# Performance work log

Hardware: AMD Instinct MI355X
Metric: run time of the kernel (lower is better)

Reference implementation:

```python
import jax, jax.numpy as jnp
import numpy as np

B = 4096; NINP = 512; NHID = 2048
NBI = 1; NBO = 8; TOPK = 4; NMRI = 2
BSO = NHID // NBO           # 256 (block_size_out)
ATT_OUT = BSO * 4           # 1024
GRU_NINP = ATT_OUT * NBO    # 8192
BSI = GRU_NINP // NBO       # 1024 (GRU per-block input size)
DK_I = 64                   # inp_att d_k (n_head=1)
NH_M = 4; DK_M = 16; DV_M = 16  # mha heads/dims


def setup_inputs() -> dict:
    key = jax.random.key(0)
    ks = jax.random.split(key, 16)
    r = lambda i, shape, s=0.01: (s * jax.random.normal(ks[i], shape)).astype(jnp.float32)
    return {
        "inp": jax.random.normal(ks[0], (B, NBI * NINP), dtype=jnp.float32),
        "hx": jax.random.normal(ks[1], (B, NHID), dtype=jnp.float32),
        "cx": jax.random.normal(ks[2], (B, NHID), dtype=jnp.float32),
        "step": 0,
        # inp_att (GroupLinear q over NBO blocks; k,v over NMRI write slots; fc out)
        "Wq_i": r(3, (NBO, BSO, DK_I)),
        "Wk_i": r(4, (NMRI, NINP, DK_I)),
        "Wv_i": r(5, (NMRI, NINP, ATT_OUT)),
        "fc_i_w": r(6, (ATT_OUT, ATT_OUT), 0.02),
        "fc_i_b": jnp.zeros((ATT_OUT,), jnp.float32),
        # mha (communication attention among blocks)
        "Wq_m": r(7, (NBO, BSO, NH_M * DK_M)),
        "Wk_m": r(8, (NBO, BSO, NH_M * DK_M)),
        "Wv_m": r(9, (NBO, BSO, NH_M * DV_M)),
        "fc_m_w": r(10, (NH_M * DV_M, BSO), 0.05),
        "fc_m_b": jnp.zeros((BSO,), jnp.float32),
        "gate_m_w": r(11, (NH_M * DV_M, BSO), 0.05),
        "gate_m_b": jnp.zeros((BSO,), jnp.float32),
        # block-diagonal GRU cell (blockified params: only diagonal blocks kept)
        "Wih": r(12, (NBO, 3 * BSO, BSI), 0.02),
        "Whh": r(13, (NBO, 3 * BSO, BSO), 0.02),
        "bih": jnp.zeros((NBO, 3 * BSO), jnp.float32),
        "bhh": jnp.zeros((NBO, 3 * BSO), jnp.float32),
    }


def _forward(inp, hx, cx, Wq_i, Wk_i, Wv_i, fc_i_w, fc_i_b, Wq_m, Wk_m, Wv_m,
             fc_m_w, fc_m_b, gate_m_w, gate_m_b, Wih, Whh, bih, bhh):
    b = inp.shape[0]
    # --- build read slots: slot 0 = zeros (null), slot 1 = input ---
    x = inp.reshape(b, NBI, NINP)
    x = jnp.tile(x, (1, NMRI - 1, 1))
    x = jnp.concatenate([jnp.zeros_like(x[:, :1]), x], axis=1)            # (b, NMRI, ninp)
    hx3 = hx.reshape(b, NBO, BSO)
    # --- inp_att: n_head=1, residual=False (gate_fc unused); Sparse_attention no-op (topk>=len_k) ---
    q = jnp.einsum('bni,nio->bno', hx3, Wq_i)                             # (b, NBO, DK_I)
    k = jnp.einsum('bni,nio->bno', x, Wk_i)                               # (b, NMRI, DK_I)
    v = jnp.einsum('bni,nio->bno', x, Wv_i)                               # (b, NMRI, ATT_OUT)
    iatt = jax.nn.softmax(jnp.einsum('bqd,bkd->bqk', q, k) / float(np.sqrt(DK_I)), axis=-1)
    inp_use = jnp.einsum('bqk,bkv->bqv', iatt, v)                         # (b, NBO, ATT_OUT)
    inp_use = (inp_use @ fc_i_w + fc_i_b).reshape(b, NBO * ATT_OUT)
    # --- top-k block mask: zero out the (NBO-TOPK) blocks most attentive to the null slot ---
    drop_idx = jax.lax.top_k(iatt[:, :, 0], NBO - TOPK)[1]                # (b, NBO-TOPK)
    mask = jnp.ones((b, NBO), inp.dtype).at[jnp.arange(b)[:, None], drop_idx].set(0.0)
    mask = jax.lax.stop_gradient(mask)                                    # mask.detach()
    mask_w = jnp.repeat(mask[:, :, None], BSO, axis=2).reshape(b, NHID)
    # --- block-diagonal GRUCell: h' = (1-z)*n + z*h ---
    x3 = inp_use.reshape(b, NBO, BSI)
    gx = jnp.einsum('bki,koi->bko', x3, Wih) + bih                        # (b, NBO, 3*BSO)
    gh = jnp.einsum('bkj,koj->bko', hx3, Whh) + bhh
    xr, xz, xn = jnp.split(gx, 3, axis=-1)
    hr, hz, hn = jnp.split(gh, 3, axis=-1)
    r = jax.nn.sigmoid(xr + hr)
    z = jax.nn.sigmoid(xz + hz)
    n = jnp.tanh(xn + r * hn)
    h_new = (1.0 - z) * n + z * hx3                                       # (b, NBO, BSO)
    # --- step attention among blocks; blocked_grad = identity fwd, grad*mask bwd ---
    m3 = mask[:, :, None]
    hg = m3 * h_new + jax.lax.stop_gradient((1.0 - m3) * h_new)
    qm = jnp.einsum('bni,nio->bno', hg, Wq_m).reshape(b, NBO, NH_M, DK_M)
    km = jnp.einsum('bni,nio->bno', hg, Wk_m).reshape(b, NBO, NH_M, DK_M)
    vm = jnp.einsum('bni,nio->bno', hg, Wv_m).reshape(b, NBO, NH_M, DV_M)
    am = jax.nn.softmax(jnp.einsum('bqhd,bkhd->bhqk', qm, km) / float(np.sqrt(DK_M)), axis=-1)
    om = jnp.einsum('bhqk,bkhd->bqhd', am, vm).reshape(b, NBO, NH_M * DV_M)
    att = jax.nn.sigmoid(om @ gate_m_w + gate_m_b) * jnp.tanh(om @ fc_m_w + fc_m_b)  # residual=True gating
    h_new = (h_new + att).reshape(b, NHID)
    # --- gated state update (GRU: cx_new = hx_new) ---
    hx_out = mask_w * h_new + (1.0 - mask_w) * hx
    cx_out = mask_w * h_new + (1.0 - mask_w) * cx
    return hx_out, cx_out, mask_w


def reference(inp, hx, cx, step, Wq_i, Wk_i, Wv_i, fc_i_w, fc_i_b, Wq_m, Wk_m, Wv_m,
              fc_m_w, fc_m_b, gate_m_w, gate_m_b, Wih, Whh, bih, bhh):
    del step  # unused by the math
    return _forward(inp, hx, cx, Wq_i, Wk_i, Wv_i, fc_i_w, fc_i_b, Wq_m, Wk_m, Wv_m,
                    fc_m_w, fc_m_b, gate_m_w, gate_m_b, Wih, Whh, bih, bhh)
```

## Files before the change

### kernel.cpp

```cpp
#include <hip/hip_runtime.h>
#include <hip/hip_bf16.h>

#define B_SZ 4096
#define NHID_ 2048

typedef __bf16 bf16x8 __attribute__((ext_vector_type(8)));
typedef float f32x4 __attribute__((ext_vector_type(4)));

__device__ __forceinline__ float sigmoidf_(float x) { return 1.f / (1.f + expf(-x)); }

#define GLDS16(gp, lp) __builtin_amdgcn_global_load_lds( \
    (const __attribute__((address_space(1))) void*)(gp), \
    (__attribute__((address_space(3))) void*)(lp), 16, 0, 0)

__global__ __launch_bounds__(256) void prep_all(
    const float* __restrict__ Wih, const float* __restrict__ fc_i_b,
    const float* __restrict__ bih, __hip_bfloat16* __restrict__ Wihb,
    float* __restrict__ cb,
    const float* __restrict__ inp, __hip_bfloat16* __restrict__ inpb,
    const float* __restrict__ Whh, __hip_bfloat16* __restrict__ Whhb,
    const float* __restrict__ WvBsrc, __hip_bfloat16* __restrict__ WvB,
    const float* __restrict__ fc_i_w, __hip_bfloat16* __restrict__ fcT,
    const float* __restrict__ Wq_m, const float* __restrict__ Wk_m,
    const float* __restrict__ Wv_m, __hip_bfloat16* __restrict__ WmT,
    const float* __restrict__ fc_m_w, const float* __restrict__ gate_m_w,
    __hip_bfloat16* __restrict__ fcgT)
{
    __shared__ float smem[32 * 33];
    const int bid = blockIdx.x;
    const int tid = threadIdx.x;

    if (bid < 6144) {
        long j = bid;
        const float* row = Wih + j * 1024;
        __hip_bfloat16* drow = Wihb + j * 1024;
        int i = tid * 4;
        float4 v = *(const float4*)(row + i);
        __hip_bfloat16 b0 = __float2bfloat16(v.x);
        __hip_bfloat16 b1 = __float2bfloat16(v.y);
        __hip_bfloat16 b2 = __float2bfloat16(v.z);
        __hip_bfloat16 b3 = __float2bfloat16(v.w);
        ushort4 u;
        u.x = *(unsigned short*)&b0; u.y = *(unsigned short*)&b1;
        u.z = *(unsigned short*)&b2; u.w = *(unsigned short*)&b3;
        *(ushort4*)(drow + i) = u;
        float s = fc_i_b[i] * v.x + fc_i_b[i + 1] * v.y +
                  fc_i_b[i + 2] * v.z + fc_i_b[i + 3] * v.w;
#pragma unroll
        for (int off = 32; off > 0; off >>= 1) s += __shfl_xor(s, off, 64);
        if ((tid & 63) == 0) smem[tid >> 6] = s;
        __syncthreads();
        if (tid == 0) cb[j] = smem[0] + smem[1] + smem[2] + smem[3] + bih[j];
    } else if (bid < 10240) {
        long i = (long)(bid - 6144) * 256 + tid;
        const float* src; __hip_bfloat16* dst; long off;
        if (i < 524288)       { src = inp;    dst = inpb; off = i; }
        else if (i < 917504)  { src = Whh;    dst = Whhb; off = i - 524288; }
        else                  { src = WvBsrc; dst = WvB;  off = i - 917504; }
        float4 v = ((const float4*)src)[off];
        __hip_bfloat16 b0 = __float2bfloat16(v.x);
        __hip_bfloat16 b1 = __float2bfloat16(v.y);
        __hip_bfloat16 b2 = __float2bfloat16(v.z);
        __hip_bfloat16 b3 = __float2bfloat16(v.w);
        ushort4 u;
        u.x = *(unsigned short*)&b0; u.y = *(unsigned short*)&b1;
        u.z = *(unsigned short*)&b2; u.w = *(unsigned short*)&b3;
        ((ushort4*)dst)[off] = u;
    } else if (bid < 11264) {
        int lb = bid - 10240;
        int r0 = (lb >> 5) * 32, c0 = (lb & 31) * 32;
        int tx = tid & 31, ty = tid >> 5;
        float (*tile)[33] = (float(*)[33])smem;
#pragma unroll
        for (int i = 0; i < 4; ++i)
            tile[ty + i * 8][tx] = fc_i_w[(long)(r0 + ty + i * 8) * 1024 + c0 + tx];
        __syncthreads();
#pragma unroll
        for (int i = 0; i < 4; ++i)
            fcT[(long)(c0 + ty + i * 8) * 1024 + r0 + tx] =
                __float2bfloat16(tile[tx][ty + i * 8]);
    } else if (bid < 11648) {
        int lb = bid - 11264;
        int z = lb >> 4, rem = lb & 15;
        int by = rem >> 1, bx = rem & 1;
        int which = z >> 3, nb = z & 7;
        const float* src = (which == 0) ? Wq_m : (which == 1) ? Wk_m : Wv_m;
        src += (long)nb * 16384;
        __hip_bfloat16* dst = WmT + (long)nb * 49152 + which * 64 * 256;
        int r0 = by * 32, c0 = bx * 32;
        int tx = tid & 31, ty = tid >> 5;
        float (*tile)[33] = (float(*)[33])smem;
#pragma unroll
        for (int i = 0; i < 4; ++i)
            tile[ty + i * 8][tx] = src[(long)(r0 + ty + i * 8) * 64 + c0 + tx];
        __syncthreads();
#pragma unroll
        for (int i = 0; i < 4; ++i)
            dst[(long)(c0 + ty + i * 8) * 256 + r0 + tx] =
                __float2bfloat16(tile[tx][ty + i * 8]);
    } else {
        int t = (bid - 11648) * 256 + tid;
        int np = t >> 6, k = t & 63;
        int o = (np >> 5) * 16 + (np & 15);
        const float* src = ((np >> 4) & 1) ? gate_m_w : fc_m_w;
        fcgT[t] = __float2bfloat16(src[k * 256 + o]);
    }
}

#define GM_BM 64
#define GM_BN 64
#define GM_BK 16

__global__ __launch_bounds__(256) void gemm_nn(
    const float* __restrict__ A, const float* __restrict__ Bm, float* __restrict__ C,
    int M, int N, int K, int lda, int ldb, int ldc,
    long sA, long sB, long sC)
{
    const int z = blockIdx.z;
    A += (long)z * sA; Bm += (long)z * sB; C += (long)z * sC;
    const int m0 = blockIdx.y * GM_BM;
    const int n0 = blockIdx.x * GM_BN;
    const int tid = threadIdx.x;
    const int tx = tid & 15;
    const int ty = tid >> 4;

    __shared__ float As[GM_BK][GM_BM + 4];
    __shared__ float Bs[GM_BK][GM_BN + 4];

    float acc[4][4] = {};

    for (int k0 = 0; k0 < K; k0 += GM_BK) {
#pragma unroll
        for (int i = 0; i < 4; ++i) {
            int idx = tid + i * 256;
            int r = idx >> 4, c = idx & 15;
            As[c][r] = A[(long)(m0 + r) * lda + k0 + c];
        }
#pragma unroll
        for (int i = 0; i < 4; ++i) {
            int idx = tid + i * 256;
            int r = idx >> 6, c = idx & 63;
            Bs[r][c] = Bm[(long)(k0 + r) * ldb + n0 + c];
        }
        __syncthreads();
#pragma unroll
        for (int kk = 0; kk < GM_BK; ++kk) {
            float4 a4 = *(const float4*)&As[kk][ty * 4];
            float4 b4 = *(const float4*)&Bs[kk][tx * 4];
            float av[4] = {a4.x, a4.y, a4.z, a4.w};
            float bv[4] = {b4.x, b4.y, b4.z, b4.w};
#pragma unroll
            for (int i = 0; i < 4; ++i)
#pragma unroll
                for (int j = 0; j < 4; ++j)
                    acc[i][j] += av[i] * bv[j];
        }
        __syncthreads();
    }
#pragma unroll
    for (int i = 0; i < 4; ++i) {
        long m = m0 + ty * 4 + i;
#pragma unroll
        for (int j = 0; j < 4; ++j) {
            int n = n0 + tx * 4 + j;
            C[m * ldc + n] = acc[i][j];
        }
    }
}

__global__ __launch_bounds__(256) void gemm_nt_f32(
    const float* __restrict__ A, int lda,
    const float* __restrict__ BT, int ldb,
    float* __restrict__ C, int ldc, int K, long sB, long sC)
{
    BT += (long)blockIdx.z * sB;
    C  += (long)blockIdx.z * sC;
    const int m0 = blockIdx.y * 64;
    const int n0 = blockIdx.x * 64;
    const int tid = threadIdx.x;
    const int tx = tid & 15;
    const int ty = tid >> 4;

    __shared__ float As[16][68];
    __shared__ float Bs[64][17];

    float acc[4][4] = {};

    for (int k0 = 0; k0 < K; k0 += 16) {
#pragma unroll
        for (int i = 0; i < 4; ++i) {
            int idx = tid + i * 256;
            int r = idx >> 4, c = idx & 15;
            As[c][r] = A[(long)(m0 + r) * lda + k0 + c];
        }
#pragma unroll
        for (int i = 0; i < 4; ++i) {
            int idx = tid + i * 256;
            int r = idx >> 4, c = idx & 15;
            Bs[r][c] = BT[(long)(n0 + r) * ldb + k0 + c];
        }
        __syncthreads();
#pragma unroll
        for (int kk = 0; kk < 16; ++kk) {
            float4 a4 = *(const float4*)&As[kk][ty * 4];
            float av[4] = {a4.x, a4.y, a4.z, a4.w};
            float bv[4];
#pragma unroll
            for (int j = 0; j < 4; ++j) bv[j] = Bs[tx * 4 + j][kk];
#pragma unroll
            for (int i = 0; i < 4; ++i)
#pragma unroll
                for (int j = 0; j < 4; ++j)
                    acc[i][j] += av[i] * bv[j];
        }
        __syncthreads();
    }
#pragma unroll
    for (int i = 0; i < 4; ++i) {
        long m = m0 + ty * 4 + i;
#pragma unroll
        for (int j = 0; j < 4; ++j) {
            int n = n0 + tx * 4 + j;
            C[m * ldc + n] = acc[i][j];
        }
    }
}

__global__ __launch_bounds__(256) void s1_mask_fused(
    const float* __restrict__ hx,
    const float* __restrict__ p,
    float* __restrict__ a_buf, float* __restrict__ mask_buf,
    __hip_bfloat16* __restrict__ hxb)
{
    const int wave = threadIdx.x >> 6;
    const int lane = threadIdx.x & 63;
    const long b = (long)blockIdx.x * 4 + wave;
    const long base = b * 2048 + lane * 4;
    float s1v[8];
#pragma unroll
    for (int n = 0; n < 8; ++n) {
        float4 hv = *(const float4*)(hx + base + n * 256);
        float4 pv = *(const float4*)(p + base + n * 256);
        __hip_bfloat16 c0 = __float2bfloat16(hv.x);
        __hip_bfloat16 c1 = __float2bfloat16(hv.y);
        __hip_bfloat16 c2 = __float2bfloat16(hv.z);
        __hip_bfloat16 c3 = __float2bfloat16(hv.w);
        ushort4 u;
        u.x = *(unsigned short*)&c0; u.y = *(unsigned short*)&c1;
        u.z = *(unsigned short*)&c2; u.w = *(unsigned short*)&c3;
        *(ushort4*)(hxb + base + n * 256) = u;
        float s = hv.x * pv.x + hv.y * pv.y + hv.z * pv.z + hv.w * pv.w;
#pragma unroll
        for (int off = 32; off > 0; off >>= 1) s += __shfl_xor(s, off, 64);
        s1v[n] = s * 0.125f;
    }
    unsigned maskbits = 0;
#pragma unroll
    for (int n = 0; n < 8; ++n) {
        int rank = 0;
#pragma unroll
        for (int m = 0; m < 8; ++m) {
            if (m == n) continue;
            if (s1v[m] < s1v[n] || (s1v[m] == s1v[n] && m < n)) rank++;
        }
        if (rank >= 4) maskbits |= (1u << n);
    }
    if (lane < 8) {
        float sv = s1v[0];
#pragma unroll
        for (int n = 1; n < 8; ++n)
            if (lane == n) sv = s1v[n];
        a_buf[b * 8 + lane] = sigmoidf_(sv);
        mask_buf[b * 8 + lane] = ((maskbits >> lane) & 1u) ? 1.0f : 0.0f;
    }
}

__global__ __launch_bounds__(256) void gemm_mfma_obf16(
    const __hip_bfloat16* __restrict__ A, int lda,
    const __hip_bfloat16* __restrict__ BT, int ldb,
    __hip_bfloat16* __restrict__ C, int ldc, int K)
{
    const int m0 = blockIdx.y * 128;
    const int n0 = blockIdx.x * 64;
    const int tid = threadIdx.x;
    const int lane = tid & 63, wid = tid >> 6;
    const int wr = wid >> 1, wc = wid & 1;
    const int l15 = lane & 15, l4 = lane >> 4;

    __shared__ __align__(16) char lds_raw[16384 + 8192];
    char* Alds = lds_raw;
    char* Blds = lds_raw + 16384;

    f32x4 acc[4][2] = {};

    for (int k0 = 0; k0 < K; k0 += 64) {
#pragma unroll
        for (int ii = 0; ii < 4; ++ii) {
            int issue = ii * 4 + wid;
            int chunk = issue * 64 + lane;
            int r = chunk >> 3, cs = chunk & 7;
            int cl = cs ^ (r & 7);
            const __hip_bfloat16* g = A + (long)(m0 + r) * lda + k0 + cl * 8;
            GLDS16(g, Alds + issue * 1024);
        }
#pragma unroll
        for (int jj = 0; jj < 2; ++jj) {
            int issue = jj * 4 + wid;
            int chunk = issue * 64 + lane;
            int r = chunk >> 3, cs = chunk & 7;
            int cl = cs ^ (r & 7);
            const __hip_bfloat16* g = BT + (long)(n0 + r) * ldb + k0 + cl * 8;
            GLDS16(g, Blds + issue * 1024);
        }
        __syncthreads();
#pragma unroll
        for (int kk = 0; kk < 2; ++kk) {
            bf16x8 af[4], bfr[2];
#pragma unroll
            for (int im = 0; im < 4; ++im) {
                int r = wr * 64 + im * 16 + l15;
                int cl = (kk * 4 + l4) ^ (l15 & 7);
                af[im] = *(const bf16x8*)(Alds + r * 128 + cl * 16);
            }
#pragma unroll
            for (int jn = 0; jn < 2; ++jn) {
                int r = wc * 32 + jn * 16 + l15;
                int cl = (kk * 4 + l4) ^ (l15 & 7);
                bfr[jn] = *(const bf16x8*)(Blds + r * 128 + cl * 16);
            }
#pragma unroll
            for (int im = 0; im < 4; ++im)
#pragma unroll
                for (int jn = 0; jn < 2; ++jn)
                    acc[im][jn] = __builtin_amdgcn_mfma_f32_16x16x32_bf16(
                        af[im], bfr[jn], acc[im][jn], 0, 0, 0);
        }
        __syncthreads();
    }
#pragma unroll
    for (int im = 0; im < 4; ++im)
#pragma unroll
        for (int reg = 0; reg < 4; ++reg) {
            long m = m0 + wr * 64 + im * 16 + l4 * 4 + reg;
#pragma unroll
            for (int jn = 0; jn < 2; ++jn) {
                int n = n0 + wc * 32 + jn * 16 + l15;
                C[m * ldc + n] = __float2bfloat16(acc[im][jn][reg]);
            }
        }
}

__global__ __launch_bounds__(256) void gemm_mfma_qkv(
    const __hip_bfloat16* __restrict__ hnewb,
    const __hip_bfloat16* __restrict__ WmT,
    __hip_bfloat16* __restrict__ qout)
{
    const int z = blockIdx.z;
    const int m0 = blockIdx.y * 128;
    const int n0 = blockIdx.x * 64;
    const int tid = threadIdx.x;
    const int lane = tid & 63, wid = tid >> 6;
    const int wr = wid >> 1, wc = wid & 1;
    const int l15 = lane & 15, l4 = lane >> 4;

    const __hip_bfloat16* A = hnewb + z * 256;
    const __hip_bfloat16* BT = WmT + (long)z * 192 * 256;

    __shared__ __align__(16) char lds_raw[16384 + 8192];
    char* Alds = lds_raw;
    char* Blds = lds_raw + 16384;

    f32x4 acc[4][2] = {};

    for (int k0 = 0; k0 < 256; k0 += 64) {
#pragma unroll
        for (int ii = 0; ii < 4; ++ii) {
            int issue = ii * 4 + wid;
            int chunk = issue * 64 + lane;
            int r = chunk >> 3, cs = chunk & 7;
            int cl = cs ^ (r & 7);
            const __hip_bfloat16* g = A + (long)(m0 + r) * 2048 + k0 + cl * 8;
            GLDS16(g, Alds + issue * 1024);
        }
#pragma unroll
        for (int jj = 0; jj < 2; ++jj) {
            int issue = jj * 4 + wid;
            int chunk = issue * 64 + lane;
            int r = chunk >> 3, cs = chunk & 7;
            int cl = cs ^ (r & 7);
            const __hip_bfloat16* g = BT + (long)(n0 + r) * 256 + k0 + cl * 8;
            GLDS16(g, Blds + issue * 1024);
        }
        __syncthreads();
#pragma unroll
        for (int kk = 0; kk < 2; ++kk) {
            bf16x8 af[4], bfr[2];
#pragma unroll
            for (int im = 0; im < 4; ++im) {
                int r = wr * 64 + im * 16 + l15;
                int cl = (kk * 4 + l4) ^ (l15 & 7);
                af[im] = *(const bf16x8*)(Alds + r * 128 + cl * 16);
            }
#pragma unroll
            for (int jn = 0; jn < 2; ++jn) {
                int r = wc * 32 + jn * 16 + l15;
                int cl = (kk * 4 + l4) ^ (l15 & 7);
                bfr[jn] = *(const bf16x8*)(Blds + r * 128 + cl * 16);
            }
#pragma unroll
            for (int im = 0; im < 4; ++im)
#pragma unroll
                for (int jn = 0; jn < 2; ++jn)
                    acc[im][jn] = __builtin_amdgcn_mfma_f32_16x16x32_bf16(
                        af[im], bfr[jn], acc[im][jn], 0, 0, 0);
        }
        __syncthreads();
    }
#pragma unroll
    for (int jn = 0; jn < 2; ++jn) {
        int j = n0 + wc * 32 + jn * 16 + l15;
        int g = j >> 6, d = j & 63;
        __hip_bfloat16* outp = qout + (long)g * 2097152 + (long)z * 64 + d;
#pragma unroll
        for (int im = 0; im < 4; ++im)
#pragma unroll
            for (int reg = 0; reg < 4; ++reg) {
                long m = m0 + wr * 64 + im * 16 + l4 * 4 + reg;
                outp[m * 512] = __float2bfloat16(acc[im][jn][reg]);
            }
    }
}

__global__ __launch_bounds__(512) void gru_fused_mfma(
    const __hip_bfloat16* __restrict__ wfcb,
    const __hip_bfloat16* __restrict__ hxb,
    const float* __restrict__ a_buf,
    const float* __restrict__ cb,
    const __hip_bfloat16* __restrict__ Wihb,
    const __hip_bfloat16* __restrict__ Whhb,
    const float* __restrict__ bhh,
    __hip_bfloat16* __restrict__ hnewb)
{
    const int bid = blockIdx.x;
    const int kblk = bid & 7;
    const int r_ = bid >> 3;
    const int ol0 = (r_ & 7) * 32;
    const int m0 = (r_ >> 3) * 128;
    const int tid = threadIdx.x;
    const int lane = tid & 63, wid = tid >> 6;
    const int wr = wid >> 1;
    const int wc = wid & 1;
    const int l15 = lane & 15, l4 = lane >> 4;

    __shared__ __align__(16) char lds_raw[2 * 28672];

    f32x4 accx[2][3] = {};
    f32x4 acch[2][3] = {};

    const __hip_bfloat16* Wk = Wihb + (long)kblk * 768 * 1024;
    const __hip_bfloat16* Wh = Whhb + (long)kblk * 768 * 256;
    const __hip_bfloat16* hxk = hxb + kblk * 256;

    const int iiA0 = wid, iiA1 = wid + 8;
    const int cA0 = iiA0 * 64 + lane, rA0 = cA0 >> 3, clA0 = (cA0 & 7) ^ (rA0 & 7);
    const int cA1 = iiA1 * 64 + lane, rA1 = cA1 >> 3, clA1 = (cA1 & 7) ^ (rA1 & 7);
    const int jjB0 = wid, jjB1 = wid + 8;
    const int cB0 = jjB0 * 64 + lane, rB0 = cB0 >> 3, clB0 = (cB0 & 7) ^ (rB0 & 7);
    const int cB1 = jjB1 * 64 + lane, rB1 = cB1 >> 3, clB1 = (cB1 & 7) ^ (rB1 & 7);
    const bool hasB1 = (wid < 4);
    const int gg0 = rB0 >> 5, oll0 = rB0 & 31;
    const int gg1 = (rB1 >> 5) & 3, oll1 = rB1 & 31;
    const int dA0 = iiA0 * 1024, dA1 = iiA1 * 1024;
    const int dB0 = 16384 + jjB0 * 1024, dB1 = 16384 + jjB1 * 1024;

    const __hip_bfloat16* pA0 = wfcb + (long)(m0 + rA0) * 1024 + clA0 * 8;
    const __hip_bfloat16* pA1 = wfcb + (long)(m0 + rA1) * 1024 + clA1 * 8;
    const __hip_bfloat16* pB0 = Wk + (long)(gg0 * 256 + ol0 + oll0) * 1024 + clB0 * 8;
    const __hip_bfloat16* pB1 = Wk + (long)(gg1 * 256 + ol0 + oll1) * 1024 + clB1 * 8;

#define STAGE4(buf) do {                                                       \
    char* L = lds_raw + (buf) * 28672;                                         \
    GLDS16(pA0, L + dA0);                                                      \
    GLDS16(pA1, L + dA1);                                                      \
    GLDS16(pB0, L + dB0);                                                      \
    if (hasB1) GLDS16(pB1, L + dB1);                                           \
    pA0 += 64; pA1 += 64; pB0 += 64; pB1 += 64;                                \
} while (0)

    int offA[2][2], offB[2][3];
#pragma unroll
    for (int kk = 0; kk < 2; ++kk) {
        int cl = (kk * 4 + l4) ^ (l15 & 7);
#pragma unroll
        for (int im = 0; im < 2; ++im)
            offA[kk][im] = (wr * 32 + im * 16 + l15) * 128 + cl * 16;
#pragma unroll
        for (int g = 0; g < 3; ++g)
            offB[kk][g] = 16384 + (g * 32 + wc * 16 + l15) * 128 + cl * 16;
    }

#define COMPUTE(acc, buf) do {                                                 \
    char* L = lds_raw + (buf) * 28672;                                         \
    _Pragma("unroll") for (int kk = 0; kk < 2; ++kk) {                         \
        bf16x8 af[2], bfr[3];                                                  \
        _Pragma("unroll") for (int im = 0; im < 2; ++im)                       \
            af[im] = *(const bf16x8*)(L + offA[kk][im]);                       \
        _Pragma("unroll") for (int g = 0; g < 3; ++g)                          \
            bfr[g] = *(const bf16x8*)(L + offB[kk][g]);                        \
        _Pragma("unroll") for (int im = 0; im < 2; ++im)                       \
            _Pragma("unroll") for (int g = 0; g < 3; ++g)                      \
                acc[im][g] = __builtin_amdgcn_mfma_f32_16x16x32_bf16(          \
                    af[im], bfr[g], acc[im][g], 0, 0, 0);                      \
    }                                                                          \
} while (0)

    STAGE4(0);
    asm volatile("s_waitcnt vmcnt(0)" ::: "memory");
    __syncthreads();

    int cur = 0;
    for (int t = 0; t < 16; ++t) {
        if (t < 15) {
            STAGE4(cur ^ 1);
        } else {
            pA0 = hxk + (long)(m0 + rA0) * 2048 + clA0 * 8;
            pA1 = hxk + (long)(m0 + rA1) * 2048 + clA1 * 8;
            pB0 = Wh + (long)(gg0 * 256 + ol0 + oll0) * 256 + clB0 * 8;
            pB1 = Wh + (long)(gg1 * 256 + ol0 + oll1) * 256 + clB1 * 8;
            STAGE4(cur ^ 1);
        }
        __builtin_amdgcn_s_setprio(1);
        COMPUTE(accx, cur);
        __builtin_amdgcn_s_setprio(0);
        asm volatile("s_waitcnt vmcnt(0)" ::: "memory");
        __syncthreads();
        cur ^= 1;
    }
    for (int t = 0; t < 4; ++t) {
        if (t < 3) STAGE4(cur ^ 1);
        __builtin_amdgcn_s_setprio(1);
        COMPUTE(acch, cur);
        __builtin_amdgcn_s_setprio(0);
        asm volatile("s_waitcnt vmcnt(0)" ::: "memory");
        __syncthreads();
        cur ^= 1;
    }
#undef STAGE4
#undef COMPUTE

    const int ol = ol0 + wc * 16 + l15;
    const float* cbk = cb + kblk * 768;
    const float cb0 = cbk[ol], cb1 = cbk[256 + ol], cb2 = cbk[512 + ol];
    const float* bhk = bhh + kblk * 768;
    const float bh0 = bhk[ol], bh1 = bhk[256 + ol], bh2 = bhk[512 + ol];
#pragma unroll
    for (int im = 0; im < 2; ++im) {
#pragma unroll
        for (int reg = 0; reg < 4; ++reg) {
            long m = m0 + wr * 32 + im * 16 + l4 * 4 + reg;
            float av = a_buf[m * 8 + kblk];
            float gx0 = av * accx[im][0][reg] + cb0;
            float gx1 = av * accx[im][1][reg] + cb1;
            float gx2 = av * accx[im][2][reg] + cb2;
            float gh0 = acch[im][0][reg] + bh0;
            float gh1 = acch[im][1][reg] + bh1;
            float gh2 = acch[im][2][reg] + bh2;
            float rr = sigmoidf_(gx0 + gh0);
            float zz = sigmoidf_(gx1 + gh1);
            float nn = tanhf(gx2 + rr * gh2);
            long idx = m * 2048 + kblk * 256 + ol;
            float hxv = __bfloat162float(hxb[idx]);
            hnewb[idx] = __float2bfloat16((1.f - zz) * nn + zz * hxv);
        }
    }
}

__global__ __launch_bounds__(256) void mattn_kernel(
    const __hip_bfloat16* __restrict__ qm, const __hip_bfloat16* __restrict__ km,
    const __hip_bfloat16* __restrict__ vm, __hip_bfloat16* __restrict__ omb)
{
    const int t = threadIdx.x;
    const int local = t & 31;
    const long b = (long)blockIdx.x * 8 + (t >> 5);
    const int h = local >> 3, qn = local & 7;
    const long base = b * 512 + h * 16;

    float qv[16];
#pragma unroll
    for (int i = 0; i < 2; ++i) {
        bf16x8 v = *(const bf16x8*)(qm + base + qn * 64 + i * 8);
#pragma unroll
        for (int j = 0; j < 8; ++j) qv[i * 8 + j] = (float)v[j];
    }
    float sc[8];
#pragma unroll
    for (int kn = 0; kn < 8; ++kn) {
        float s = 0.f;
#pragma unroll
        for (int i = 0; i < 2; ++i) {
            bf16x8 v = *(const bf16x8*)(km + base + kn * 64 + i * 8);
#pragma unroll
            for (int j = 0; j < 8; ++j) s += qv[i * 8 + j] * (float)v[j];
        }
        sc[kn] = s * 0.25f;
    }
    float mx = sc[0];
#pragma unroll
    for (int kn = 1; kn < 8; ++kn) mx = fmaxf(mx, sc[kn]);
    float ssum = 0.f;
#pragma unroll
    for (int kn = 0; kn < 8; ++kn) { sc[kn] = expf(sc[kn] - mx); ssum += sc[kn]; }
    float inv = 1.f / ssum;

    float acc[16] = {};
#pragma unroll
    for (int kn = 0; kn < 8; ++kn) {
        float w = sc[kn] * inv;
#pragma unroll
        for (int i = 0; i < 2; ++i) {
            bf16x8 v = *(const bf16x8*)(vm + base + kn * 64 + i * 8);
#pragma unroll
            for (int j = 0; j < 8; ++j) acc[i * 8 + j] += w * (float)v[j];
        }
    }
#pragma unroll
    for (int i = 0; i < 2; ++i) {
        bf16x8 o;
#pragma unroll
        for (int j = 0; j < 8; ++j) o[j] = (__bf16)acc[i * 8 + j];
        *(bf16x8*)(omb + base + qn * 64 + i * 8) = o;
    }
}

__global__ __launch_bounds__(256) void att_final(
    const __hip_bfloat16* __restrict__ omb,
    const __hip_bfloat16* __restrict__ fcgT,
    const float* __restrict__ fc_b, const float* __restrict__ gate_b,
    const __hip_bfloat16* __restrict__ hnewb,
    const float* __restrict__ maskb,
    const float* __restrict__ hx, const float* __restrict__ cx,
    float* __restrict__ hx_out, float* __restrict__ cx_out,
    float* __restrict__ mask_w)
{
    const int m0 = blockIdx.y * 128;
    const int n0 = blockIdx.x * 64;
    const int tid = threadIdx.x;
    const int lane = tid & 63, wid = tid >> 6;
    const int wr = wid >> 1, wc = wid & 1;
    const int l15 = lane & 15, l4 = lane >> 4;

    __shared__ __align__(16) char lds_raw[16384 + 8192];
    char* Alds = lds_raw;
    char* Blds = lds_raw + 16384;

    f32x4 acc[4][2] = {};
#pragma unroll
    for (int ii = 0; ii < 4; ++ii) {
        int issue = ii * 4 + wid;
        int chunk = issue * 64 + lane;
        int r = chunk >> 3, cs = chunk & 7;
        int cl = cs ^ (r & 7);
        const __hip_bfloat16* g = omb + (long)(m0 + r) * 64 + cl * 8;
        GLDS16(g, Alds + issue * 1024);
    }
#pragma unroll
    for (int jj = 0; jj < 2; ++jj) {
        int issue = jj * 4 + wid;
        int chunk = issue * 64 + lane;
        int r = chunk >> 3, cs = chunk & 7;
        int cl = cs ^ (r & 7);
        const __hip_bfloat16* g = fcgT + (long)(n0 + r) * 64 + cl * 8;
        GLDS16(g, Blds + issue * 1024);
    }
    __syncthreads();
#pragma unroll
    for (int kk = 0; kk < 2; ++kk) {
        bf16x8 af[4], bfr[2];
#pragma unroll
        for (int im = 0; im < 4; ++im) {
            int r = wr * 64 + im * 16 + l15;
            int cl = (kk * 4 + l4) ^ (l15 & 7);
            af[im] = *(const bf16x8*)(Alds + r * 128 + cl * 16);
        }
#pragma unroll
        for (int jn = 0; jn < 2; ++jn) {
            int r = wc * 32 + jn * 16 + l15;
            int cl = (kk * 4 + l4) ^ (l15 & 7);
            bfr[jn] = *(const bf16x8*)(Blds + r * 128 + cl * 16);
        }
#pragma unroll
        for (int im = 0; im < 4; ++im)
#pragma unroll
            for (int jn = 0; jn < 2; ++jn)
                acc[im][jn] = __builtin_amdgcn_mfma_f32_16x16x32_bf16(
                    af[im], bfr[jn], acc[im][jn], 0, 0, 0);
    }
    const int o = ((n0 + wc * 32) >> 1) + l15;
    const float fb = fc_b[o], gb = gate_b[o];
#pragma unroll
    for (int im = 0; im < 4; ++im)
#pragma unroll
        for (int reg = 0; reg < 4; ++reg) {
            long m = m0 + wr * 64 + im * 16 + l4 * 4 + reg;
            long idx = m * 256 + o;
            float mv = maskb[m];
            float att = sigmoidf_(acc[im][1][reg] + gb) * tanhf(acc[im][0][reg] + fb);
            float ho, co;
            if (mv != 0.f) {
                float h2 = __bfloat162float(hnewb[idx]) + att;
                ho = h2; co = h2;
            } else {
                ho = hx[idx]; co = cx[idx];
            }
            hx_out[idx] = ho;
            cx_out[idx] = co;
            mask_w[idx] = mv;
        }
}

extern "C" void kernel_launch(void* const* d_in, const int* in_sizes, int n_in,
                              void* d_out, int out_size, void* d_ws, size_t ws_size,
                              hipStream_t stream)
{
    const float* inp     = (const float*)d_in[0];
    const float* hx      = (const float*)d_in[1];
    const float* cx      = (const float*)d_in[2];
    const float* Wq_i    = (const float*)d_in[4];
    const float* Wk_i    = (const float*)d_in[5];
    const float* Wv_i    = (const float*)d_in[6];
    const float* fc_i_w  = (const float*)d_in[7];
    const float* fc_i_b  = (const float*)d_in[8];
    const float* Wq_m    = (const float*)d_in[9];
    const float* Wk_m    = (const float*)d_in[10];
    const float* Wv_m    = (const float*)d_in[11];
    const float* fc_m_w  = (const float*)d_in[12];
    const float* fc_m_b  = (const float*)d_in[13];
    const float* gate_m_w= (const float*)d_in[14];
    const float* gate_m_b= (const float*)d_in[15];
    const float* Wih     = (const float*)d_in[16];
    const float* Whh     = (const float*)d_in[17];
    const float* bih     = (const float*)d_in[18];
    const float* bhh     = (const float*)d_in[19];

    float* out = (float*)d_out;
    const long BH = (long)B_SZ * NHID_;
    float* hx_out = out;
    float* cx_out = out + BH;
    float* mask_w = out + 2 * BH;
    __hip_bfloat16* hxb = (__hip_bfloat16*)out;
    __hip_bfloat16* qkvb = (__hip_bfloat16*)out;
    float* pbuf = cx_out;

    float* w = (float*)d_ws;
    float* a_buf = w;
    float* maskb = w + 32768;
    float* cbuf  = w + 65536;
    __hip_bfloat16* fcgT = (__hip_bfloat16*)(w + 73728);
    __hip_bfloat16* WmT  = (__hip_bfloat16*)(w + 90112);
    __hip_bfloat16* Wihb = (__hip_bfloat16*)(w + 286720);
    __hip_bfloat16* Whhb = (__hip_bfloat16*)(w + 3432448);
    __hip_bfloat16* wfcb = (__hip_bfloat16*)(w + 4218880);
    __hip_bfloat16* hnewb= (__hip_bfloat16*)(w + 6316032);
    float* krow = w + 8413184;
    __hip_bfloat16* inpb = (__hip_bfloat16*)(w + 8675328);
    __hip_bfloat16* WvB  = (__hip_bfloat16*)(w + 9723904);
    __hip_bfloat16* fcT  = (__hip_bfloat16*)(w + 9986048);
    __hip_bfloat16* WvFT = (__hip_bfloat16*)(w + 10510336);
    __hip_bfloat16* omb  = (__hip_bfloat16*)(w + 286720);

    prep_all<<<dim3(11776), dim3(256), 0, stream>>>(
        Wih, fc_i_b, bih, Wihb, cbuf,
        inp, inpb, Whh, Whhb, Wv_i + 512 * 1024, WvB,
        fc_i_w, fcT, Wq_m, Wk_m, Wv_m, WmT, fc_m_w, gate_m_w, fcgT);
    gemm_nn<<<dim3(1, 64, 1), dim3(256), 0, stream>>>(
        inp, Wk_i + 512 * 64, krow, 4096, 64, 512, 512, 64, 64, 0, 0, 0);
    gemm_nt_f32<<<dim3(4, 64, 8), dim3(256), 0, stream>>>(
        krow, 64, Wq_i, 64, pbuf, 2048, 64, 16384, 256);
    s1_mask_fused<<<dim3(1024), dim3(256), 0, stream>>>(hx, pbuf, a_buf, maskb, hxb);
    gemm_mfma_obf16<<<dim3(8, 8, 1), dim3(256), 0, stream>>>(
        fcT, 1024, WvB, 1024, WvFT, 512, 1024);
    gemm_mfma_obf16<<<dim3(16, 32, 1), dim3(256), 0, stream>>>(
        inpb, 512, WvFT, 512, wfcb, 1024, 512);
    gru_fused_mfma<<<dim3(2048), dim3(512), 0, stream>>>(
        wfcb, hxb, a_buf, cbuf, Wihb, Whhb, bhh, hnewb);
    gemm_mfma_qkv<<<dim3(3, 32, 8), dim3(256), 0, stream>>>(hnewb, WmT, qkvb);
    mattn_kernel<<<dim3(512), dim3(256), 0, stream>>>(
        qkvb, qkvb + 2097152, qkvb + 4194304, omb);
    att_final<<<dim3(8, 256, 1), dim3(256), 0, stream>>>(
        omb, fcgT, fc_m_b, gate_m_b, hnewb, maskb, hx, cx, hx_out, cx_out, mask_w);
}
```

Baseline: 255.0 us.

## Fold attention value/fc projection into GRU input weights, shrinking GRU K dimension

Precomputes the product of the per-block GRU input weights with the combined Wv·fc projection, giving weights of shape 768x512 per block. The GRU then multiplies the 512-wide bf16 input directly instead of the 1024-wide fc output. This removes the large B×1024 activation GEMM and halves the K loop in the fused GRU kernel. In exchange, a weight-only batched GEMM runs each call, and the pre-multiplied weights are rounded to bf16, which changes numerical error. The workspace layout is also reshuffled to fit the new buffers.

```diff
diff --git a/kernel.cpp b/kernel.cpp
--- a/kernel.cpp
+++ b/kernel.cpp
@@ -278,8 +278,12 @@
 __global__ __launch_bounds__(256) void gemm_mfma_obf16(
     const __hip_bfloat16* __restrict__ A, int lda,
     const __hip_bfloat16* __restrict__ BT, int ldb,
-    __hip_bfloat16* __restrict__ C, int ldc, int K)
-{
+    __hip_bfloat16* __restrict__ C, int ldc, int K,
+    long sA, long sB, long sC)
+{
+    A  += (long)blockIdx.z * sA;
+    BT += (long)blockIdx.z * sB;
+    C  += (long)blockIdx.z * sC;
     const int m0 = blockIdx.y * 128;
     const int n0 = blockIdx.x * 64;
     const int tid = threadIdx.x;
@@ -432,11 +436,11 @@
 }
 
 __global__ __launch_bounds__(512) void gru_fused_mfma(
-    const __hip_bfloat16* __restrict__ wfcb,
+    const __hip_bfloat16* __restrict__ inpb,
     const __hip_bfloat16* __restrict__ hxb,
     const float* __restrict__ a_buf,
     const float* __restrict__ cb,
-    const __hip_bfloat16* __restrict__ Wihb,
+    const __hip_bfloat16* __restrict__ W2T,
     const __hip_bfloat16* __restrict__ Whhb,
     const float* __restrict__ bhh,
     __hip_bfloat16* __restrict__ hnewb)
@@ -457,7 +461,7 @@
     f32x4 accx[2][3] = {};
     f32x4 acch[2][3] = {};
 
-    const __hip_bfloat16* Wk = Wihb + (long)kblk * 768 * 1024;
+    const __hip_bfloat16* W2 = W2T + (long)kblk * 768 * 512;
     const __hip_bfloat16* Wh = Whhb + (long)kblk * 768 * 256;
     const __hip_bfloat16* hxk = hxb + kblk * 256;
 
@@ -473,10 +477,10 @@
     const int dA0 = iiA0 * 1024, dA1 = iiA1 * 1024;
     const int dB0 = 16384 + jjB0 * 1024, dB1 = 16384 + jjB1 * 1024;
 
-    const __hip_bfloat16* pA0 = wfcb + (long)(m0 + rA0) * 1024 + clA0 * 8;
-    const __hip_bfloat16* pA1 = wfcb + (long)(m0 + rA1) * 1024 + clA1 * 8;
-    const __hip_bfloat16* pB0 = Wk + (long)(gg0 * 256 + ol0 + oll0) * 1024 + clB0 * 8;
-    const __hip_bfloat16* pB1 = Wk + (long)(gg1 * 256 + ol0 + oll1) * 1024 + clB1 * 8;
+    const __hip_bfloat16* pA0 = inpb + (long)(m0 + rA0) * 512 + clA0 * 8;
+    const __hip_bfloat16* pA1 = inpb + (long)(m0 + rA1) * 512 + clA1 * 8;
+    const __hip_bfloat16* pB0 = W2 + (long)(gg0 * 256 + ol0 + oll0) * 512 + clB0 * 8;
+    const __hip_bfloat16* pB1 = W2 + (long)(gg1 * 256 + ol0 + oll1) * 512 + clB1 * 8;
 
 #define STAGE4(buf) do {                                                       \
     char* L = lds_raw + (buf) * 28672;                                         \
@@ -519,8 +523,8 @@
     __syncthreads();
 
     int cur = 0;
-    for (int t = 0; t < 16; ++t) {
-        if (t < 15) {
+    for (int t = 0; t < 8; ++t) {
+        if (t < 7) {
             STAGE4(cur ^ 1);
         } else {
             pA0 = hxk + (long)(m0 + rA0) * 2048 + clA0 * 8;
@@ -758,15 +762,15 @@
     __hip_bfloat16* fcgT = (__hip_bfloat16*)(w + 73728);
     __hip_bfloat16* WmT  = (__hip_bfloat16*)(w + 90112);
     __hip_bfloat16* Wihb = (__hip_bfloat16*)(w + 286720);
-    __hip_bfloat16* Whhb = (__hip_bfloat16*)(w + 3432448);
-    __hip_bfloat16* wfcb = (__hip_bfloat16*)(w + 4218880);
-    __hip_bfloat16* hnewb= (__hip_bfloat16*)(w + 6316032);
-    float* krow = w + 8413184;
-    __hip_bfloat16* inpb = (__hip_bfloat16*)(w + 8675328);
-    __hip_bfloat16* WvB  = (__hip_bfloat16*)(w + 9723904);
-    __hip_bfloat16* fcT  = (__hip_bfloat16*)(w + 9986048);
-    __hip_bfloat16* WvFT = (__hip_bfloat16*)(w + 10510336);
-    __hip_bfloat16* omb  = (__hip_bfloat16*)(w + 286720);
+    __hip_bfloat16* fcT  = (__hip_bfloat16*)(w + 3432448);
+    __hip_bfloat16* WvB  = (__hip_bfloat16*)(w + 3956736);
+    float* krow = w + 4218880;
+    __hip_bfloat16* hnewb= (__hip_bfloat16*)(w + 286720);
+    __hip_bfloat16* WvFTt= (__hip_bfloat16*)(w + 4481024);
+    __hip_bfloat16* inpb = (__hip_bfloat16*)(w + 4743168);
+    __hip_bfloat16* W2T  = (__hip_bfloat16*)(w + 5791744);
+    __hip_bfloat16* Whhb = (__hip_bfloat16*)(w + 7364608);
+    __hip_bfloat16* omb  = (__hip_bfloat16*)(w + 5791744);
 
     prep_all<<<dim3(11776), dim3(256), 0, stream>>>(
         Wih, fc_i_b, bih, Wihb, cbuf,
@@ -777,12 +781,13 @@
     gemm_nt_f32<<<dim3(4, 64, 8), dim3(256), 0, stream>>>(
         krow, 64, Wq_i, 64, pbuf, 2048, 64, 16384, 256);
     s1_mask_fused<<<dim3(1024), dim3(256), 0, stream>>>(hx, pbuf, a_buf, maskb, hxb);
-    gemm_mfma_obf16<<<dim3(8, 8, 1), dim3(256), 0, stream>>>(
-        fcT, 1024, WvB, 1024, WvFT, 512, 1024);
-    gemm_mfma_obf16<<<dim3(16, 32, 1), dim3(256), 0, stream>>>(
-        inpb, 512, WvFT, 512, wfcb, 1024, 512);
+    gemm_mfma_obf16<<<dim3(16, 4, 1), dim3(256), 0, stream>>>(
+        WvB, 1024, fcT, 1024, WvFTt, 1024, 1024, 0, 0, 0);
+    gemm_mfma_obf16<<<dim3(8, 6, 8), dim3(256), 0, stream>>>(
+        Wihb, 1024, WvFTt, 1024, W2T, 512, 1024,
+        768L * 1024, 0, 768L * 512);
     gru_fused_mfma<<<dim3(2048), dim3(512), 0, stream>>>(
-        wfcb, hxb, a_buf, cbuf, Wihb, Whhb, bhh, hnewb);
+        inpb, hxb, a_buf, cbuf, W2T, Whhb, bhh, hnewb);
     gemm_mfma_qkv<<<dim3(3, 32, 8), dim3(256), 0, stream>>>(hnewb, WmT, qkvb);
     mattn_kernel<<<dim3(512), dim3(256), 0, stream>>>(
         qkvb, qkvb + 2097152, qkvb + 4194304, omb);
```

After: 231.6 us. 9.1% less time.
